# Kernel tuning notes

Measured on AMD Instinct MI355X. Metric: run time of the kernel, lower is better.

The kernel has to match this reference:

```python
import jax, jax.numpy as jnp
import numpy as np

# Swin layer dims (Swin-B-ish stage): batch, height, width, channels, heads, window, shift, mlp hidden
B, H, W, C = 64, 28, 28, 512
HEADS, WS, SHIFT, MLP = 16, 7, 3, 2048
EPS = 1e-5
HD = C // HEADS            # head dim
W2 = WS * WS               # tokens per window
NW = (H // WS) * (W // WS) # windows per image


def _rel_index():
    # standard Swin relative position index for a WSxWS window -> [W2, W2] in [0, (2WS-1)^2)
    coords = np.stack(np.meshgrid(np.arange(WS), np.arange(WS), indexing='ij')).reshape(2, -1)
    rel = (coords[:, :, None] - coords[:, None, :]).transpose(1, 2, 0)
    rel[:, :, 0] += WS - 1
    rel[:, :, 1] += WS - 1
    rel[:, :, 0] *= 2 * WS - 1
    return rel.sum(-1)


def _attn_mask():
    # shifted-window additive mask, [NW, W2, W2] with 0 / -100 entries (shape-static constant)
    img = np.zeros((H, W))
    cnt = 0
    slices = (slice(0, -WS), slice(-WS, -SHIFT), slice(-SHIFT, None))
    for hs in slices:
        for ws_ in slices:
            img[hs, ws_] = cnt
            cnt += 1
    mw = img.reshape(H // WS, WS, W // WS, WS).transpose(0, 2, 1, 3).reshape(NW, W2)
    m = mw[:, None, :] - mw[:, :, None]
    return np.where(m != 0, -100.0, 0.0).astype(np.float32)


def _ln(x, g, b):
    mu = x.mean(-1, keepdims=True)
    var = ((x - mu) ** 2).mean(-1, keepdims=True)
    return (x - mu) * jax.lax.rsqrt(var + EPS) * g + b


def setup_inputs() -> dict:
    key = jax.random.key(0)
    ks = jax.random.split(key, 10)
    s = 0.02
    f32 = jnp.float32
    return {
        'x': jax.random.normal(ks[0], (B, H * W, C), f32),
        'g1': jnp.ones((C,), f32), 'b1': jnp.zeros((C,), f32),
        'wq': jax.random.normal(ks[1], (C, C), f32) * s, 'bq': jnp.zeros((C,), f32),
        'wk': jax.random.normal(ks[2], (C, C), f32) * s, 'bk': jnp.zeros((C,), f32),
        'wv': jax.random.normal(ks[3], (C, C), f32) * s, 'bv': jnp.zeros((C,), f32),
        'rel_table': jax.random.normal(ks[4], ((2 * WS - 1) ** 2, HEADS), f32) * s,
        'wo': jax.random.normal(ks[5], (C, C), f32) * s, 'bo': jnp.zeros((C,), f32),
        'g2': jnp.ones((C,), f32), 'b2': jnp.zeros((C,), f32),
        'wi': jax.random.normal(ks[6], (C, MLP), f32) * s, 'bi': jnp.zeros((MLP,), f32),
        'w_out': jax.random.normal(ks[7], (MLP, C), f32) * s, 'b_out': jnp.zeros((C,), f32),
        'rel_index': jnp.asarray(_rel_index(), jnp.int32),
    }


def reference(x, g1, b1, wq, bq, wk, bk, wv, bv, rel_table, wo, bo, g2, b2, wi, bi, w_out, b_out, rel_index):
    shortcut = x                                                    # [B, HW, C]
    h = _ln(x, g1, b1).reshape(B, H, W, C)
    # cyclic shift
    h = jnp.roll(h, (-SHIFT, -SHIFT), axis=(1, 2))
    # window partition -> [B*NW, W2, C]
    win = h.reshape(B, H // WS, WS, W // WS, WS, C).transpose(0, 1, 3, 2, 4, 5).reshape(B * NW, W2, C)
    # multi-head attention within windows
    q = (win @ wq + bq).reshape(-1, W2, HEADS, HD).transpose(0, 2, 1, 3)
    k = (win @ wk + bk).reshape(-1, W2, HEADS, HD).transpose(0, 2, 1, 3)
    v = (win @ wv + bv).reshape(-1, W2, HEADS, HD).transpose(0, 2, 1, 3)
    scores = jnp.einsum('nhid,nhjd->nhij', q, k) / jnp.sqrt(jnp.float32(HD))
    bias = rel_table[rel_index.reshape(-1)].reshape(W2, W2, HEADS).transpose(2, 0, 1)
    scores = scores + bias[None]
    mask = jnp.asarray(_attn_mask())                                # [NW, W2, W2]
    scores = scores.reshape(B, NW, HEADS, W2, W2) + mask[None, :, None]
    probs = jax.nn.softmax(scores, axis=-1).reshape(B * NW, HEADS, W2, W2)
    ctx = jnp.einsum('nhij,nhjd->nhid', probs, v).transpose(0, 2, 1, 3).reshape(B * NW, W2, C)
    attn_out = ctx @ wo + bo
    # window reverse -> [B, H, W, C]
    rev = attn_out.reshape(B, H // WS, W // WS, WS, WS, C).transpose(0, 1, 3, 2, 4, 5).reshape(B, H, W, C)
    # reverse cyclic shift
    rev = jnp.roll(rev, (SHIFT, SHIFT), axis=(1, 2))
    x1 = shortcut + rev.reshape(B, H * W, C)
    # MLP block
    h2 = _ln(x1, g2, b2)
    mid = jax.nn.gelu(h2 @ wi + bi, approximate=False)
    return x1 + (mid @ w_out + b_out)
```

## Files before the change

kernel.cpp:

```cpp
#include <hip/hip_runtime.h>
#include <cstdint>

typedef unsigned short u16;
typedef unsigned int   u32;

__device__ __forceinline__ float bf2f(u16 b) { return __uint_as_float(((u32)b) << 16); }
__device__ __forceinline__ u16 f2bf(float f) {
    u32 u = __float_as_uint(f);
    u32 r = u + 0x7fffu + ((u >> 16) & 1u);
    return (u16)(r >> 16);
}
__device__ __forceinline__ void unpack2(u32 u, float& a, float& b) {
    a = bf2f((u16)(u & 0xffffu)); b = bf2f((u16)(u >> 16));
}
__device__ __forceinline__ float ldx(const void* p, size_t i, int fl) {
    return fl ? ((const float*)p)[i] : bf2f(((const u16*)p)[i]);
}

typedef __bf16 bf16x8 __attribute__((ext_vector_type(8)));
typedef float  f32x4  __attribute__((ext_vector_type(4)));

__device__ __forceinline__ void gl16(const u16* g, u16* l) {
    __builtin_amdgcn_global_load_lds(
        (const __attribute__((address_space(1))) u32*)g,
        (__attribute__((address_space(3))) u32*)l, 16, 0, 0);
}

__global__ void detect_k(const u16* __restrict__ wq, int* __restrict__ flag) {
    if (threadIdx.x == 0 && blockIdx.x == 0) {
        int bad = 0;
        for (int i = 0; i < 256; i++) {
            float v = fabsf(bf2f(wq[i]));
            if (!(v == 0.f || (v > 1e-30f && v < 1e3f))) bad++;
        }
        *flag = (bad >= 32) ? 1 : 0;
    }
}

__global__ void transp_k(const void* __restrict__ s, u16* __restrict__ d, int R, int Cc,
                         const int* __restrict__ flag) {
    int fl = *flag;
    int e = blockIdx.x * 256 + threadIdx.x;
    if (e < R * Cc) {
        int r = e / Cc, c = e - r * Cc;
        d[(size_t)c * R + r] = fl ? f2bf(((const float*)s)[e]) : ((const u16*)s)[e];
    }
}

__global__ void tabm_k(const void* __restrict__ rel_table, const int* __restrict__ rel_index,
                       float* __restrict__ tabm, const int* __restrict__ flag) {
    int fl = *flag;
    int e = blockIdx.x * 256 + threadIdx.x;
    int p = e >> 12;
    int rem = e & 4095;
    int i = rem >> 6, l = (rem >> 2) & 15, ni = rem & 3;
    int j = ni * 16 + l;
    int nw = p >> 4, h = p & 15;
    float v = -30000.f;
    if (i < 49 && j < 49) {
        v = ldx(rel_table, (size_t)rel_index[i * 49 + j] * 16 + h, fl);
        int wy = (nw >> 2) * 7, wx = (nw & 3) * 7;
        int yi = wy + i / 7, xi = wx + i % 7;
        int yj = wy + j / 7, xj = wx + j % 7;
        int ri = (yi < 21 ? 0 : (yi < 25 ? 1 : 2)) * 3 + (xi < 21 ? 0 : (xi < 25 ? 1 : 2));
        int rj = (yj < 21 ? 0 : (yj < 25 ? 1 : 2)) * 3 + (xj < 21 ? 0 : (xj < 25 ? 1 : 2));
        if (ri != rj) v -= 100.f;
    }
    tabm[e] = v;
}

__global__ __launch_bounds__(256) void ln_win_k(const void* __restrict__ x,
        const void* __restrict__ g, const void* __restrict__ be, u16* __restrict__ win,
        const int* __restrict__ flag) {
    int fl = *flag;
    int lane = threadIdx.x & 63;
    int t = blockIdx.x * 4 + (threadIdx.x >> 6);
    int w = t / 49, p = t - w * 49;
    int bimg = w >> 4, nw = w & 15;
    int r = p / 7, c = p - r * 7;
    int hs = (nw >> 2) * 7 + r, wsx = (nw & 3) * 7 + c;
    int ho = hs + 3; if (ho >= 28) ho -= 28;
    int wo = wsx + 3; if (wo >= 28) wo -= 28;
    size_t base = ((size_t)bimg * 784 + (size_t)ho * 28 + wo) * 512 + lane * 8;
    float f[8];
    if (fl) {
        const float4* src = (const float4*)((const float*)x + base);
        float4 v0 = src[0], v1 = src[1];
        f[0]=v0.x; f[1]=v0.y; f[2]=v0.z; f[3]=v0.w; f[4]=v1.x; f[5]=v1.y; f[6]=v1.z; f[7]=v1.w;
    } else {
        uint4 u = *(const uint4*)((const u16*)x + base);
        unpack2(u.x, f[0], f[1]); unpack2(u.y, f[2], f[3]);
        unpack2(u.z, f[4], f[5]); unpack2(u.w, f[6], f[7]);
    }
    float s = 0.f, q = 0.f;
#pragma unroll
    for (int j = 0; j < 8; j++) { s += f[j]; q += f[j] * f[j]; }
#pragma unroll
    for (int o = 32; o; o >>= 1) { s += __shfl_xor(s, o, 64); q += __shfl_xor(q, o, 64); }
    float mean = s * (1.f / 512.f);
    float rstd = rsqrtf(q * (1.f / 512.f) - mean * mean + 1e-5f);
    u32 o[4];
#pragma unroll
    for (int j = 0; j < 4; j++) {
        float g0 = ldx(g, lane * 8 + 2 * j, fl),     b0 = ldx(be, lane * 8 + 2 * j, fl);
        float g1v = ldx(g, lane * 8 + 2 * j + 1, fl), b1v = ldx(be, lane * 8 + 2 * j + 1, fl);
        float y0 = (f[2 * j] - mean) * rstd * g0 + b0;
        float y1 = (f[2 * j + 1] - mean) * rstd * g1v + b1v;
        o[j] = (u32)f2bf(y0) | ((u32)f2bf(y1) << 16);
    }
    *(uint4*)(win + (size_t)t * 512 + lane * 8) = make_uint4(o[0], o[1], o[2], o[3]);
}

__global__ __launch_bounds__(256) void ln2_k(const float* __restrict__ x1,
        const void* __restrict__ g, const void* __restrict__ be, u16* __restrict__ h2,
        const int* __restrict__ flag) {
    int fl = *flag;
    int lane = threadIdx.x & 63;
    int t = blockIdx.x * 4 + (threadIdx.x >> 6);
    const float4* src = (const float4*)(x1 + (size_t)t * 512 + lane * 8);
    float4 v0 = src[0], v1 = src[1];
    float f[8] = {v0.x, v0.y, v0.z, v0.w, v1.x, v1.y, v1.z, v1.w};
    float s = 0.f, q = 0.f;
#pragma unroll
    for (int j = 0; j < 8; j++) { s += f[j]; q += f[j] * f[j]; }
#pragma unroll
    for (int o = 32; o; o >>= 1) { s += __shfl_xor(s, o, 64); q += __shfl_xor(q, o, 64); }
    float mean = s * (1.f / 512.f);
    float rstd = rsqrtf(q * (1.f / 512.f) - mean * mean + 1e-5f);
    u32 o[4];
#pragma unroll
    for (int j = 0; j < 4; j++) {
        float g0 = ldx(g, lane * 8 + 2 * j, fl),     b0 = ldx(be, lane * 8 + 2 * j, fl);
        float g1v = ldx(g, lane * 8 + 2 * j + 1, fl), b1v = ldx(be, lane * 8 + 2 * j + 1, fl);
        float y0 = (f[2 * j] - mean) * rstd * g0 + b0;
        float y1 = (f[2 * j + 1] - mean) * rstd * g1v + b1v;
        o[j] = (u32)f2bf(y0) | ((u32)f2bf(y1) << 16);
    }
    *(uint4*)(h2 + (size_t)t * 512 + lane * 8) = make_uint4(o[0], o[1], o[2], o[3]);
}

template <int MODE>
__global__ __launch_bounds__(256) void gemm_bt(
        const u16* __restrict__ A, const u16* __restrict__ BT, const void* __restrict__ bias,
        int M, int N, int K, float alpha,
        void* __restrict__ outv, float* __restrict__ outf,
        const void* __restrict__ resb, const float* __restrict__ resf, int m_off,
        const int* __restrict__ flag) {
    __shared__ __align__(16) u16 As[128 * 32];
    __shared__ __align__(16) u16 Bs[128 * 32];
    int fl = *flag;
    int tid = threadIdx.x;
    int wave = tid >> 6, lane = tid & 63;
    int l15 = lane & 15, quad = lane >> 4;
    int wm = (wave & 1) << 6, wn = (wave >> 1) << 6;
    int m0 = blockIdx.y * 128, n0 = blockIdx.x * 128;

    int srow0 = wave * 16 + (lane >> 2);
    int srow1 = srow0 + 64;
    int scol = (lane & 3) * 8;
    const u16* a0 = A + (size_t)(m0 + srow0) * K + scol;
    const u16* a1 = A + (size_t)(m0 + srow1) * K + scol;
    const u16* b0 = BT + (size_t)(n0 + srow0) * K + scol;
    const u16* b1 = BT + (size_t)(n0 + srow1) * K + scol;
    u16* lA0 = &As[wave * 16 * 32];
    u16* lA1 = &As[(wave + 4) * 16 * 32];
    u16* lB0 = &Bs[wave * 16 * 32];
    u16* lB1 = &Bs[(wave + 4) * 16 * 32];

    f32x4 acc[4][4];
#pragma unroll
    for (int mi = 0; mi < 4; mi++)
#pragma unroll
        for (int ni = 0; ni < 4; ni++) acc[mi][ni] = (f32x4){0.f, 0.f, 0.f, 0.f};

    for (int k0 = 0; k0 < K; k0 += 32) {
        gl16(a0, lA0); gl16(a1, lA1); gl16(b0, lB0); gl16(b1, lB1);
        a0 += 32; a1 += 32; b0 += 32; b1 += 32;
        __syncthreads();
        bf16x8 af[4], bfm[4];
#pragma unroll
        for (int mi = 0; mi < 4; mi++)
            af[mi] = *(const bf16x8*)&As[(wm + mi * 16 + l15) * 32 + quad * 8];
#pragma unroll
        for (int ni = 0; ni < 4; ni++)
            bfm[ni] = *(const bf16x8*)&Bs[(wn + ni * 16 + l15) * 32 + quad * 8];
#pragma unroll
        for (int mi = 0; mi < 4; mi++)
#pragma unroll
            for (int ni = 0; ni < 4; ni++)
                acc[mi][ni] = __builtin_amdgcn_mfma_f32_16x16x32_bf16(af[mi], bfm[ni], acc[mi][ni], 0, 0, 0);
        __syncthreads();
    }

#pragma unroll
    for (int mi = 0; mi < 4; mi++) {
#pragma unroll
        for (int r = 0; r < 4; r++) {
            int gm = m0 + wm + mi * 16 + quad * 4 + r;
            size_t obase = 0;
            if constexpr (MODE == 1) {
                int w = gm / 49, p = gm - w * 49;
                int bimg = w >> 4, nw = w & 15;
                int rr = p / 7, cc = p - rr * 7;
                int hs = (nw >> 2) * 7 + rr, wsx = (nw & 3) * 7 + cc;
                int ho = hs + 3; if (ho >= 28) ho -= 28;
                int wo2 = wsx + 3; if (wo2 >= 28) wo2 -= 28;
                obase = ((size_t)bimg * 784 + (size_t)ho * 28 + wo2) * 512;
            }
#pragma unroll
            for (int ni = 0; ni < 4; ni++) {
                int gn = n0 + wn + ni * 16 + l15;
                float v = acc[mi][ni][r] + ldx(bias, gn, fl);
                if constexpr (MODE == 0) {
                    ((u16*)outv)[(size_t)gm * N + gn] = f2bf(v * alpha);
                } else if constexpr (MODE == 1) {
                    size_t oi = obase + gn;
                    outf[oi] = v + ldx(resb, oi, fl);
                } else if constexpr (MODE == 2) {
                    ((u16*)outv)[(size_t)gm * N + gn] = f2bf(0.5f * v * (1.f + erff(v * 0.70710678118f)));
                } else {
                    size_t oi = (size_t)(m_off + gm) * 512 + gn;
                    float y = v + resf[oi];
                    if (fl) ((float*)outv)[oi] = y; else ((u16*)outv)[oi] = f2bf(y);
                }
            }
        }
    }
}

__global__ __launch_bounds__(64) void attn_mfma_k(const u16* __restrict__ qb,
        const u16* __restrict__ kb, const u16* __restrict__ vb,
        const float* __restrict__ tabm, u16* __restrict__ ctx) {
    __shared__ __align__(16) u16 Ps[64 * 72];
    __shared__ __align__(16) u16 Vs[32 * 72];
    int bid = blockIdx.x;
    int w = bid >> 4, h = bid & 15, nw = w & 15;
    int lane = threadIdx.x;
    int l15 = lane & 15, quad = lane >> 4;
    size_t base = (size_t)w * 49 * 512 + h * 32;

    {
        int j = lane < 49 ? lane : 48;
        const u16* vr = vb + base + (size_t)j * 512;
        u16 vv[32];
        *(uint4*)&vv[0]  = *(const uint4*)(vr);
        *(uint4*)&vv[8]  = *(const uint4*)(vr + 8);
        *(uint4*)&vv[16] = *(const uint4*)(vr + 16);
        *(uint4*)&vv[24] = *(const uint4*)(vr + 24);
#pragma unroll
        for (int d = 0; d < 32; d++) Vs[d * 72 + lane] = vv[d];
    }

    bf16x8 qf[4], kf[4];
#pragma unroll
    for (int t = 0; t < 4; t++) {
        int rq = t * 16 + l15; rq = rq < 49 ? rq : 48;
        qf[t] = *(const bf16x8*)(qb + base + (size_t)rq * 512 + quad * 8);
        kf[t] = *(const bf16x8*)(kb + base + (size_t)rq * 512 + quad * 8);
    }
    f32x4 acc[4][4];
#pragma unroll
    for (int mi = 0; mi < 4; mi++)
#pragma unroll
        for (int ni = 0; ni < 4; ni++) acc[mi][ni] = (f32x4){0.f, 0.f, 0.f, 0.f};
#pragma unroll
    for (int mi = 0; mi < 4; mi++)
#pragma unroll
        for (int ni = 0; ni < 4; ni++)
            acc[mi][ni] = __builtin_amdgcn_mfma_f32_16x16x32_bf16(qf[mi], kf[ni], acc[mi][ni], 0, 0, 0);

    const float* tb = tabm + (size_t)(nw * 16 + h) * 4096;
#pragma unroll
    for (int mi = 0; mi < 4; mi++) {
#pragma unroll
        for (int r = 0; r < 4; r++) {
            int i = mi * 16 + quad * 4 + r;
            float4 t = *(const float4*)(tb + i * 64 + l15 * 4);
            float s0 = acc[mi][0][r] + t.x;
            float s1 = acc[mi][1][r] + t.y;
            float s2 = acc[mi][2][r] + t.z;
            float s3 = acc[mi][3][r] + t.w;
            float mx = fmaxf(fmaxf(s0, s1), fmaxf(s2, s3));
#pragma unroll
            for (int o = 8; o; o >>= 1) mx = fmaxf(mx, __shfl_xor(mx, o, 64));
            float p0 = __expf(s0 - mx), p1 = __expf(s1 - mx);
            float p2 = __expf(s2 - mx), p3 = __expf(s3 - mx);
            float sum = p0 + p1 + p2 + p3;
#pragma unroll
            for (int o = 8; o; o >>= 1) sum += __shfl_xor(sum, o, 64);
            float inv = 1.f / sum;
            Ps[i * 72 +  0 + l15] = f2bf(p0 * inv);
            Ps[i * 72 + 16 + l15] = f2bf(p1 * inv);
            Ps[i * 72 + 32 + l15] = f2bf(p2 * inv);
            Ps[i * 72 + 48 + l15] = f2bf(p3 * inv);
        }
    }
    __syncthreads();

    f32x4 oacc[4][2];
#pragma unroll
    for (int mi = 0; mi < 4; mi++)
#pragma unroll
        for (int ni = 0; ni < 2; ni++) oacc[mi][ni] = (f32x4){0.f, 0.f, 0.f, 0.f};
#pragma unroll
    for (int ks = 0; ks < 2; ks++) {
        bf16x8 pf[4], vf[2];
#pragma unroll
        for (int mi = 0; mi < 4; mi++)
            pf[mi] = *(const bf16x8*)&Ps[(mi * 16 + l15) * 72 + ks * 32 + quad * 8];
#pragma unroll
        for (int ni = 0; ni < 2; ni++)
            vf[ni] = *(const bf16x8*)&Vs[(ni * 16 + l15) * 72 + ks * 32 + quad * 8];
#pragma unroll
        for (int mi = 0; mi < 4; mi++)
#pragma unroll
            for (int ni = 0; ni < 2; ni++)
                oacc[mi][ni] = __builtin_amdgcn_mfma_f32_16x16x32_bf16(pf[mi], vf[ni], oacc[mi][ni], 0, 0, 0);
    }

#pragma unroll
    for (int mi = 0; mi < 4; mi++) {
#pragma unroll
        for (int r = 0; r < 4; r++) {
            int i = mi * 16 + quad * 4 + r;
            if (i < 49) {
                ctx[base + (size_t)i * 512 + l15]      = f2bf(oacc[mi][0][r]);
                ctx[base + (size_t)i * 512 + 16 + l15] = f2bf(oacc[mi][1][r]);
            }
        }
    }
}

extern "C" void kernel_launch(void* const* d_in, const int* in_sizes, int n_in,
                              void* d_out, int out_size, void* d_ws, size_t ws_size,
                              hipStream_t stream) {
    const void* x   = d_in[0];
    const void* g1  = d_in[1];
    const void* b1  = d_in[2];
    const void* wq  = d_in[3];
    const void* bq  = d_in[4];
    const void* wk  = d_in[5];
    const void* bk  = d_in[6];
    const void* wv  = d_in[7];
    const void* bv  = d_in[8];
    const void* rel_table = d_in[9];
    const void* wo  = d_in[10];
    const void* bo  = d_in[11];
    const void* g2  = d_in[12];
    const void* b2  = d_in[13];
    const void* wi  = d_in[14];
    const void* bi  = d_in[15];
    const void* wout = d_in[16];
    const void* bout = d_in[17];
    const int* rel_index = (const int*)d_in[18];

    char* ws = (char*)d_ws;
    const size_t SZ = (size_t)50176 * 512 * 2;
    u16*   win = (u16*)(ws);
    u16*   qb  = (u16*)(ws + SZ);
    u16*   kb  = (u16*)(ws + 2 * SZ);
    u16*   vb  = (u16*)(ws + 3 * SZ);
    u16*   ctx = win;
    float* x1  = (float*)(ws + SZ);
    u16*   h2  = vb;
    u16*   mid = (u16*)(ws + 4 * SZ);
    float* tabm = (float*)(ws + 4 * SZ);
    u16*   wt  = (u16*)(ws + 5 * SZ);
    u16*   wqT = wt;
    u16*   wkT = wt + 262144;
    u16*   wvT = wt + 524288;
    u16*   woT = wt + 786432;
    u16*   wiT = wt + 1048576;
    u16*   woutT = wt + 2097152;
    int*   flag = (int*)(ws + 5 * SZ + 6291456);

    detect_k<<<1, 64, 0, stream>>>((const u16*)wq, flag);

    transp_k<<<1024, 256, 0, stream>>>(wq, wqT, 512, 512, flag);
    transp_k<<<1024, 256, 0, stream>>>(wk, wkT, 512, 512, flag);
    transp_k<<<1024, 256, 0, stream>>>(wv, wvT, 512, 512, flag);
    transp_k<<<1024, 256, 0, stream>>>(wo, woT, 512, 512, flag);
    transp_k<<<4096, 256, 0, stream>>>(wi, wiT, 512, 2048, flag);
    transp_k<<<4096, 256, 0, stream>>>(wout, woutT, 2048, 512, flag);
    tabm_k<<<4096, 256, 0, stream>>>(rel_table, rel_index, tabm, flag);

    ln_win_k<<<12544, 256, 0, stream>>>(x, g1, b1, win, flag);

    dim3 gq(4, 392);
    gemm_bt<0><<<gq, 256, 0, stream>>>(win, wqT, bq, 50176, 512, 512, 0.1767766953f,
                                       qb, nullptr, nullptr, nullptr, 0, flag);
    gemm_bt<0><<<gq, 256, 0, stream>>>(win, wkT, bk, 50176, 512, 512, 1.f,
                                       kb, nullptr, nullptr, nullptr, 0, flag);
    gemm_bt<0><<<gq, 256, 0, stream>>>(win, wvT, bv, 50176, 512, 512, 1.f,
                                       vb, nullptr, nullptr, nullptr, 0, flag);

    attn_mfma_k<<<16384, 64, 0, stream>>>(qb, kb, vb, tabm, ctx);

    gemm_bt<1><<<gq, 256, 0, stream>>>(ctx, woT, bo, 50176, 512, 512, 1.f,
                                       nullptr, x1, x, nullptr, 0, flag);

    ln2_k<<<12544, 256, 0, stream>>>(x1, g2, b2, h2, flag);

    for (int c = 0; c < 4; c++) {
        dim3 g1m(16, 98), g2m(4, 98);
        gemm_bt<2><<<g1m, 256, 0, stream>>>(h2 + (size_t)c * 12544 * 512, wiT, bi,
                                            12544, 2048, 512, 1.f,
                                            mid, nullptr, nullptr, nullptr, 0, flag);
        gemm_bt<3><<<g2m, 256, 0, stream>>>(mid, woutT, bout,
                                            12544, 512, 2048, 1.f,
                                            d_out, nullptr, nullptr, x1, c * 12544, flag);
    }
}
```

Baseline: 1.451 ms.

## Fuse QKV projections and restructure GEMMs around a row-resident A tile

Concatenates the Q, K and V weights into one 1536-wide GEMM so the LayerNorm output is read once, and folds the attention scale into the transposed Q weights and a packed bias buffer. The GEMM is rewritten: each block keeps a 64x512 slice of A in LDS and each wave streams its 128 output columns of B directly from global memory, instead of using double-LDS-staged 128x128 tiles. Attention reads from the interleaved QKV buffer. This cuts launches and A reloads, but loses LDS reuse of B and greatly lowers the block count and occupancy, especially for the MLP GEMMs.

```diff
diff --git a/kernel.cpp b/kernel.cpp
--- a/kernel.cpp
+++ b/kernel.cpp
@@ -19,12 +19,6 @@
 
 typedef __bf16 bf16x8 __attribute__((ext_vector_type(8)));
 typedef float  f32x4  __attribute__((ext_vector_type(4)));
-
-__device__ __forceinline__ void gl16(const u16* g, u16* l) {
-    __builtin_amdgcn_global_load_lds(
-        (const __attribute__((address_space(1))) u32*)g,
-        (__attribute__((address_space(3))) u32*)l, 16, 0, 0);
-}
 
 __global__ void detect_k(const u16* __restrict__ wq, int* __restrict__ flag) {
     if (threadIdx.x == 0 && blockIdx.x == 0) {
@@ -38,13 +32,29 @@
 }
 
 __global__ void transp_k(const void* __restrict__ s, u16* __restrict__ d, int R, int Cc,
-                         const int* __restrict__ flag) {
+                         float alpha, const int* __restrict__ flag) {
     int fl = *flag;
     int e = blockIdx.x * 256 + threadIdx.x;
     if (e < R * Cc) {
         int r = e / Cc, c = e - r * Cc;
-        d[(size_t)c * R + r] = fl ? f2bf(((const float*)s)[e]) : ((const u16*)s)[e];
-    }
+        d[(size_t)c * R + r] = f2bf(ldx(s, e, fl) * alpha);
+    }
+}
+
+__global__ void bpack_k(const void* bq, const void* bk, const void* bv, const void* bo,
+                        const void* bi, const void* bout, u16* __restrict__ bcat,
+                        const int* __restrict__ flag) {
+    int fl = *flag;
+    int e = blockIdx.x * 256 + threadIdx.x;
+    float v;
+    if      (e < 512)  v = ldx(bq, e, fl) * 0.1767766953f;
+    else if (e < 1024) v = ldx(bk, e - 512, fl);
+    else if (e < 1536) v = ldx(bv, e - 1024, fl);
+    else if (e < 2048) v = ldx(bo, e - 1536, fl);
+    else if (e < 4096) v = ldx(bi, e - 2048, fl);
+    else if (e < 4608) v = ldx(bout, e - 4096, fl);
+    else return;
+    bcat[e] = f2bf(v);
 }
 
 __global__ void tabm_k(const void* __restrict__ rel_table, const int* __restrict__ rel_index,
@@ -140,85 +150,121 @@
 }
 
 template <int MODE>
-__global__ __launch_bounds__(256) void gemm_bt(
-        const u16* __restrict__ A, const u16* __restrict__ BT, const void* __restrict__ bias,
-        int M, int N, int K, float alpha,
+__global__ __launch_bounds__(256) void gemm_ar(
+        const u16* __restrict__ A, const u16* __restrict__ BT, const u16* __restrict__ biasb,
+        int M, int N, int K,
         void* __restrict__ outv, float* __restrict__ outf,
         const void* __restrict__ resb, const float* __restrict__ resf, int m_off,
         const int* __restrict__ flag) {
-    __shared__ __align__(16) u16 As[128 * 32];
-    __shared__ __align__(16) u16 Bs[128 * 32];
-    int fl = *flag;
-    int tid = threadIdx.x;
-    int wave = tid >> 6, lane = tid & 63;
+    __shared__ __align__(16) u16 As[64 * 520];
+    int fl = *flag;
+    int tid = threadIdx.x, wave = tid >> 6, lane = tid & 63;
     int l15 = lane & 15, quad = lane >> 4;
-    int wm = (wave & 1) << 6, wn = (wave >> 1) << 6;
-    int m0 = blockIdx.y * 128, n0 = blockIdx.x * 128;
-
-    int srow0 = wave * 16 + (lane >> 2);
-    int srow1 = srow0 + 64;
-    int scol = (lane & 3) * 8;
-    const u16* a0 = A + (size_t)(m0 + srow0) * K + scol;
-    const u16* a1 = A + (size_t)(m0 + srow1) * K + scol;
-    const u16* b0 = BT + (size_t)(n0 + srow0) * K + scol;
-    const u16* b1 = BT + (size_t)(n0 + srow1) * K + scol;
-    u16* lA0 = &As[wave * 16 * 32];
-    u16* lA1 = &As[(wave + 4) * 16 * 32];
-    u16* lB0 = &Bs[wave * 16 * 32];
-    u16* lB1 = &Bs[(wave + 4) * 16 * 32];
-
-    f32x4 acc[4][4];
-#pragma unroll
-    for (int mi = 0; mi < 4; mi++)
-#pragma unroll
-        for (int ni = 0; ni < 4; ni++) acc[mi][ni] = (f32x4){0.f, 0.f, 0.f, 0.f};
-
-    for (int k0 = 0; k0 < K; k0 += 32) {
-        gl16(a0, lA0); gl16(a1, lA1); gl16(b0, lB0); gl16(b1, lB1);
-        a0 += 32; a1 += 32; b0 += 32; b1 += 32;
+    int m0 = blockIdx.x * 64;
+
+    if constexpr (MODE != 3) {
+#pragma unroll 4
+        for (int i = 0; i < 16; i++) {
+            int row = i * 4 + wave;
+            *(uint4*)&As[row * 520 + lane * 8] =
+                *(const uint4*)(A + (size_t)(m0 + row) * K + lane * 8);
+        }
         __syncthreads();
-        bf16x8 af[4], bfm[4];
+
+        for (int g = wave; g < (N >> 7); g += 4) {
+            f32x4 acc[4][8];
+#pragma unroll
+            for (int mi = 0; mi < 4; mi++)
+#pragma unroll
+                for (int ni = 0; ni < 8; ni++) acc[mi][ni] = (f32x4){0.f, 0.f, 0.f, 0.f};
+
+            for (int k0 = 0; k0 < 512; k0 += 32) {
+                bf16x8 af[4], bf[8];
+#pragma unroll
+                for (int mi = 0; mi < 4; mi++)
+                    af[mi] = *(const bf16x8*)&As[(mi * 16 + l15) * 520 + k0 + quad * 8];
+#pragma unroll
+                for (int ni = 0; ni < 8; ni++)
+                    bf[ni] = *(const bf16x8*)(BT + (size_t)(g * 128 + ni * 16 + l15) * K + k0 + quad * 8);
+#pragma unroll
+                for (int mi = 0; mi < 4; mi++)
+#pragma unroll
+                    for (int ni = 0; ni < 8; ni++)
+                        acc[mi][ni] = __builtin_amdgcn_mfma_f32_16x16x32_bf16(af[mi], bf[ni], acc[mi][ni], 0, 0, 0);
+            }
+
+#pragma unroll
+            for (int mi = 0; mi < 4; mi++) {
+#pragma unroll
+                for (int r = 0; r < 4; r++) {
+                    int gm = m0 + mi * 16 + quad * 4 + r;
+                    size_t obase = 0;
+                    if constexpr (MODE == 1) {
+                        int w = gm / 49, p = gm - w * 49;
+                        int bimg = w >> 4, nw = w & 15;
+                        int rr = p / 7, cc = p - rr * 7;
+                        int hs = (nw >> 2) * 7 + rr, wsx = (nw & 3) * 7 + cc;
+                        int ho = hs + 3; if (ho >= 28) ho -= 28;
+                        int wo2 = wsx + 3; if (wo2 >= 28) wo2 -= 28;
+                        obase = ((size_t)bimg * 784 + (size_t)ho * 28 + wo2) * 512;
+                    }
+#pragma unroll
+                    for (int ni = 0; ni < 8; ni++) {
+                        int gn = g * 128 + ni * 16 + l15;
+                        float v = acc[mi][ni][r] + bf2f(biasb[gn]);
+                        if constexpr (MODE == 0) {
+                            ((u16*)outv)[(size_t)gm * N + gn] = f2bf(v);
+                        } else if constexpr (MODE == 1) {
+                            size_t oi = obase + gn;
+                            outf[oi] = v + ldx(resb, oi, fl);
+                        } else if constexpr (MODE == 2) {
+                            ((u16*)outv)[(size_t)gm * N + gn] =
+                                f2bf(0.5f * v * (1.f + erff(v * 0.70710678118f)));
+                        }
+                    }
+                }
+            }
+        }
+    } else {
+        f32x4 acc[4][8];
 #pragma unroll
         for (int mi = 0; mi < 4; mi++)
-            af[mi] = *(const bf16x8*)&As[(wm + mi * 16 + l15) * 32 + quad * 8];
-#pragma unroll
-        for (int ni = 0; ni < 4; ni++)
-            bfm[ni] = *(const bf16x8*)&Bs[(wn + ni * 16 + l15) * 32 + quad * 8];
-#pragma unroll
-        for (int mi = 0; mi < 4; mi++)
-#pragma unroll
-            for (int ni = 0; ni < 4; ni++)
-                acc[mi][ni] = __builtin_amdgcn_mfma_f32_16x16x32_bf16(af[mi], bfm[ni], acc[mi][ni], 0, 0, 0);
-        __syncthreads();
-    }
-
-#pragma unroll
-    for (int mi = 0; mi < 4; mi++) {
-#pragma unroll
-        for (int r = 0; r < 4; r++) {
-            int gm = m0 + wm + mi * 16 + quad * 4 + r;
-            size_t obase = 0;
-            if constexpr (MODE == 1) {
-                int w = gm / 49, p = gm - w * 49;
-                int bimg = w >> 4, nw = w & 15;
-                int rr = p / 7, cc = p - rr * 7;
-                int hs = (nw >> 2) * 7 + rr, wsx = (nw & 3) * 7 + cc;
-                int ho = hs + 3; if (ho >= 28) ho -= 28;
-                int wo2 = wsx + 3; if (wo2 >= 28) wo2 -= 28;
-                obase = ((size_t)bimg * 784 + (size_t)ho * 28 + wo2) * 512;
-            }
-#pragma unroll
-            for (int ni = 0; ni < 4; ni++) {
-                int gn = n0 + wn + ni * 16 + l15;
-                float v = acc[mi][ni][r] + ldx(bias, gn, fl);
-                if constexpr (MODE == 0) {
-                    ((u16*)outv)[(size_t)gm * N + gn] = f2bf(v * alpha);
-                } else if constexpr (MODE == 1) {
-                    size_t oi = obase + gn;
-                    outf[oi] = v + ldx(resb, oi, fl);
-                } else if constexpr (MODE == 2) {
-                    ((u16*)outv)[(size_t)gm * N + gn] = f2bf(0.5f * v * (1.f + erff(v * 0.70710678118f)));
-                } else {
+#pragma unroll
+            for (int ni = 0; ni < 8; ni++) acc[mi][ni] = (f32x4){0.f, 0.f, 0.f, 0.f};
+        int g = wave;
+        for (int k2 = 0; k2 < K; k2 += 512) {
+            if (k2) __syncthreads();
+#pragma unroll 4
+            for (int i = 0; i < 16; i++) {
+                int row = i * 4 + wave;
+                *(uint4*)&As[row * 520 + lane * 8] =
+                    *(const uint4*)(A + (size_t)(m0 + row) * K + k2 + lane * 8);
+            }
+            __syncthreads();
+            for (int k0 = 0; k0 < 512; k0 += 32) {
+                bf16x8 af[4], bf[8];
+#pragma unroll
+                for (int mi = 0; mi < 4; mi++)
+                    af[mi] = *(const bf16x8*)&As[(mi * 16 + l15) * 520 + k0 + quad * 8];
+#pragma unroll
+                for (int ni = 0; ni < 8; ni++)
+                    bf[ni] = *(const bf16x8*)(BT + (size_t)(g * 128 + ni * 16 + l15) * K + k2 + k0 + quad * 8);
+#pragma unroll
+                for (int mi = 0; mi < 4; mi++)
+#pragma unroll
+                    for (int ni = 0; ni < 8; ni++)
+                        acc[mi][ni] = __builtin_amdgcn_mfma_f32_16x16x32_bf16(af[mi], bf[ni], acc[mi][ni], 0, 0, 0);
+            }
+        }
+#pragma unroll
+        for (int mi = 0; mi < 4; mi++) {
+#pragma unroll
+            for (int r = 0; r < 4; r++) {
+                int gm = m0 + mi * 16 + quad * 4 + r;
+#pragma unroll
+                for (int ni = 0; ni < 8; ni++) {
+                    int gn = g * 128 + ni * 16 + l15;
+                    float v = acc[mi][ni][r] + bf2f(biasb[gn]);
                     size_t oi = (size_t)(m_off + gm) * 512 + gn;
                     float y = v + resf[oi];
                     if (fl) ((float*)outv)[oi] = y; else ((u16*)outv)[oi] = f2bf(y);
@@ -228,8 +274,7 @@
     }
 }
 
-__global__ __launch_bounds__(64) void attn_mfma_k(const u16* __restrict__ qb,
-        const u16* __restrict__ kb, const u16* __restrict__ vb,
+__global__ __launch_bounds__(64) void attn_mfma_k(const u16* __restrict__ qkv,
         const float* __restrict__ tabm, u16* __restrict__ ctx) {
     __shared__ __align__(16) u16 Ps[64 * 72];
     __shared__ __align__(16) u16 Vs[32 * 72];
@@ -237,11 +282,11 @@
     int w = bid >> 4, h = bid & 15, nw = w & 15;
     int lane = threadIdx.x;
     int l15 = lane & 15, quad = lane >> 4;
-    size_t base = (size_t)w * 49 * 512 + h * 32;
+    size_t rowb = (size_t)w * 49 * 1536 + h * 32;
 
     {
         int j = lane < 49 ? lane : 48;
-        const u16* vr = vb + base + (size_t)j * 512;
+        const u16* vr = qkv + rowb + (size_t)j * 1536 + 1024;
         u16 vv[32];
         *(uint4*)&vv[0]  = *(const uint4*)(vr);
         *(uint4*)&vv[8]  = *(const uint4*)(vr + 8);
@@ -255,8 +300,8 @@
 #pragma unroll
     for (int t = 0; t < 4; t++) {
         int rq = t * 16 + l15; rq = rq < 49 ? rq : 48;
-        qf[t] = *(const bf16x8*)(qb + base + (size_t)rq * 512 + quad * 8);
-        kf[t] = *(const bf16x8*)(kb + base + (size_t)rq * 512 + quad * 8);
+        qf[t] = *(const bf16x8*)(qkv + rowb + (size_t)rq * 1536 + quad * 8);
+        kf[t] = *(const bf16x8*)(qkv + rowb + (size_t)rq * 1536 + 512 + quad * 8);
     }
     f32x4 acc[4][4];
 #pragma unroll
@@ -318,14 +363,15 @@
                 oacc[mi][ni] = __builtin_amdgcn_mfma_f32_16x16x32_bf16(pf[mi], vf[ni], oacc[mi][ni], 0, 0, 0);
     }
 
+    size_t cb = (size_t)w * 49 * 512 + h * 32;
 #pragma unroll
     for (int mi = 0; mi < 4; mi++) {
 #pragma unroll
         for (int r = 0; r < 4; r++) {
             int i = mi * 16 + quad * 4 + r;
             if (i < 49) {
-                ctx[base + (size_t)i * 512 + l15]      = f2bf(oacc[mi][0][r]);
-                ctx[base + (size_t)i * 512 + 16 + l15] = f2bf(oacc[mi][1][r]);
+                ctx[cb + (size_t)i * 512 + l15]      = f2bf(oacc[mi][0][r]);
+                ctx[cb + (size_t)i * 512 + 16 + l15] = f2bf(oacc[mi][1][r]);
             }
         }
     }
@@ -357,57 +403,49 @@
     char* ws = (char*)d_ws;
     const size_t SZ = (size_t)50176 * 512 * 2;
     u16*   win = (u16*)(ws);
-    u16*   qb  = (u16*)(ws + SZ);
-    u16*   kb  = (u16*)(ws + 2 * SZ);
-    u16*   vb  = (u16*)(ws + 3 * SZ);
+    u16*   qkv = (u16*)(ws + SZ);
     u16*   ctx = win;
     float* x1  = (float*)(ws + SZ);
-    u16*   h2  = vb;
+    u16*   h2  = (u16*)(ws + 3 * SZ);
     u16*   mid = (u16*)(ws + 4 * SZ);
     float* tabm = (float*)(ws + 4 * SZ);
     u16*   wt  = (u16*)(ws + 5 * SZ);
-    u16*   wqT = wt;
-    u16*   wkT = wt + 262144;
-    u16*   wvT = wt + 524288;
-    u16*   woT = wt + 786432;
-    u16*   wiT = wt + 1048576;
+    u16*   wqkvT = wt;
+    u16*   woT   = wt + 786432;
+    u16*   wiT   = wt + 1048576;
     u16*   woutT = wt + 2097152;
-    int*   flag = (int*)(ws + 5 * SZ + 6291456);
+    u16*   bcat  = wt + 3145728;
+    int*   flag  = (int*)(wt + 3145728 + 8192);
 
     detect_k<<<1, 64, 0, stream>>>((const u16*)wq, flag);
 
-    transp_k<<<1024, 256, 0, stream>>>(wq, wqT, 512, 512, flag);
-    transp_k<<<1024, 256, 0, stream>>>(wk, wkT, 512, 512, flag);
-    transp_k<<<1024, 256, 0, stream>>>(wv, wvT, 512, 512, flag);
-    transp_k<<<1024, 256, 0, stream>>>(wo, woT, 512, 512, flag);
-    transp_k<<<4096, 256, 0, stream>>>(wi, wiT, 512, 2048, flag);
-    transp_k<<<4096, 256, 0, stream>>>(wout, woutT, 2048, 512, flag);
+    transp_k<<<1024, 256, 0, stream>>>(wq, wqkvT,          512, 512, 0.1767766953f, flag);
+    transp_k<<<1024, 256, 0, stream>>>(wk, wqkvT + 262144, 512, 512, 1.f, flag);
+    transp_k<<<1024, 256, 0, stream>>>(wv, wqkvT + 524288, 512, 512, 1.f, flag);
+    transp_k<<<1024, 256, 0, stream>>>(wo, woT,            512, 512, 1.f, flag);
+    transp_k<<<4096, 256, 0, stream>>>(wi, wiT,            512, 2048, 1.f, flag);
+    transp_k<<<4096, 256, 0, stream>>>(wout, woutT,        2048, 512, 1.f, flag);
+    bpack_k<<<18, 256, 0, stream>>>(bq, bk, bv, bo, bi, bout, bcat, flag);
     tabm_k<<<4096, 256, 0, stream>>>(rel_table, rel_index, tabm, flag);
 
     ln_win_k<<<12544, 256, 0, stream>>>(x, g1, b1, win, flag);
 
-    dim3 gq(4, 392);
-    gemm_bt<0><<<gq, 256, 0, stream>>>(win, wqT, bq, 50176, 512, 512, 0.1767766953f,
-                                       qb, nullptr, nullptr, nullptr, 0, flag);
-    gemm_bt<0><<<gq, 256, 0, stream>>>(win, wkT, bk, 50176, 512, 512, 1.f,
-                                       kb, nullptr, nullptr, nullptr, 0, flag);
-    gemm_bt<0><<<gq, 256, 0, stream>>>(win, wvT, bv, 50176, 512, 512, 1.f,
-                                       vb, nullptr, nullptr, nullptr, 0, flag);
-
-    attn_mfma_k<<<16384, 64, 0, stream>>>(qb, kb, vb, tabm, ctx);
-
-    gemm_bt<1><<<gq, 256, 0, stream>>>(ctx, woT, bo, 50176, 512, 512, 1.f,
-                                       nullptr, x1, x, nullptr, 0, flag);
+    gemm_ar<0><<<784, 256, 0, stream>>>(win, wqkvT, bcat, 50176, 1536, 512,
+                                        qkv, nullptr, nullptr, nullptr, 0, flag);
+
+    attn_mfma_k<<<16384, 64, 0, stream>>>(qkv, tabm, ctx);
+
+    gemm_ar<1><<<784, 256, 0, stream>>>(ctx, woT, bcat + 1536, 50176, 512, 512,
+                                        nullptr, x1, x, nullptr, 0, flag);
 
     ln2_k<<<12544, 256, 0, stream>>>(x1, g2, b2, h2, flag);
 
     for (int c = 0; c < 4; c++) {
-        dim3 g1m(16, 98), g2m(4, 98);
-        gemm_bt<2><<<g1m, 256, 0, stream>>>(h2 + (size_t)c * 12544 * 512, wiT, bi,
-                                            12544, 2048, 512, 1.f,
+        gemm_ar<2><<<196, 256, 0, stream>>>(h2 + (size_t)c * 12544 * 512, wiT, bcat + 2048,
+                                            12544, 2048, 512,
                                             mid, nullptr, nullptr, nullptr, 0, flag);
-        gemm_bt<3><<<g2m, 256, 0, stream>>>(mid, woutT, bout,
-                                            12544, 512, 2048, 1.f,
+        gemm_ar<3><<<196, 256, 0, stream>>>(mid, woutT, bcat + 4096,
+                                            12544, 512, 2048,
                                             d_out, nullptr, nullptr, x1, c * 12544, flag);
     }
 }
```

Result: slower. 1.921 ms (+32.4%).
